# Kernel tuning notes

Hardware: AMD Instinct MI355X
Metric: run time of the kernel (lower is better)

## Reference

```python
import jax, jax.numpy as jnp
import numpy as np
import math

N, D, H, E = 4096, 128, 8, 131072
HD = D // H  # head_dim = 16
SCALE = 1.0 / math.sqrt(HD)


def ln(x, g, b, eps=1e-5):
    m = x.mean(-1, keepdims=True)
    v = ((x - m) ** 2).mean(-1, keepdims=True)
    return (x - m) * jax.lax.rsqrt(v + eps) * g + b


def setup_inputs() -> dict:
    key = jax.random.key(0)
    ks = iter(jax.random.split(key, 40))

    def lin(out_d, in_d):
        w = jax.random.normal(next(ks), (out_d, in_d), jnp.float32) / math.sqrt(in_d)
        b = jnp.zeros((out_d,), jnp.float32)
        return w, b

    x = jax.random.normal(next(ks), (N, D), jnp.float32)
    edge_index = jax.random.randint(next(ks), (2, E), 0, N, dtype=jnp.int64)
    wq_l, bq_l = lin(D, D); wk_l, bk_l = lin(D, D); wv_l, bv_l = lin(D, D)
    wg, bg = lin(D, 2 * D)
    wq_g, bq_g = lin(D, D); wk_g, bk_g = lin(D, D); wv_g, bv_g = lin(D, D)
    wo_g, bo_g = lin(D, D)
    wf, bf = lin(D, 2 * D)
    gf = jnp.ones((D,), jnp.float32); betaf = jnp.zeros((D,), jnp.float32)
    w1, b1 = lin(4 * D, D); w2, b2 = lin(D, 4 * D)
    g1 = jnp.ones((D,), jnp.float32); be1 = jnp.zeros((D,), jnp.float32)
    g2 = jnp.ones((D,), jnp.float32); be2 = jnp.zeros((D,), jnp.float32)
    return dict(x=x, edge_index=edge_index,
                wq_l=wq_l, bq_l=bq_l, wk_l=wk_l, bk_l=bk_l, wv_l=wv_l, bv_l=bv_l,
                wg=wg, bg=bg,
                wq_g=wq_g, bq_g=bq_g, wk_g=wk_g, bk_g=bk_g, wv_g=wv_g, bv_g=bv_g,
                wo_g=wo_g, bo_g=bo_g,
                wf=wf, bf=bf, gf=gf, betaf=betaf,
                w1=w1, b1=b1, w2=w2, b2=b2,
                g1=g1, be1=be1, g2=g2, be2=be2)


def reference(x, edge_index, wq_l, bq_l, wk_l, bk_l, wv_l, bv_l, wg, bg,
              wq_g, bq_g, wk_g, bk_g, wv_g, bv_g, wo_g, bo_g,
              wf, bf, gf, betaf, w1, b1, w2, b2, g1, be1, g2, be2):
    src, dst = edge_index[0], edge_index[1]  # PyG: j=source, i=target
    # ---- local edge-indexed multi-head attention (GraphInteractionModule) ----
    Q = (x @ wq_l.T + bq_l).reshape(N, H, HD)
    K = (x @ wk_l.T + bk_l).reshape(N, H, HD)
    V = (x @ wv_l.T + bv_l).reshape(N, H, HD)
    attn = (Q[dst] * K[src]).sum(-1) * SCALE            # [E, H]
    m = jax.ops.segment_max(attn, dst, num_segments=N)  # [N, H]
    e = jnp.exp(attn - m[dst])
    s = jax.ops.segment_sum(e, dst, num_segments=N)
    alpha = e / s[dst]                                  # segment softmax over edges into each dst
    agg = jax.ops.segment_sum(V[src] * alpha[..., None], dst, num_segments=N).reshape(N, D)
    gate = jax.nn.sigmoid(jnp.concatenate([x, agg], axis=-1) @ wg.T + bg)
    local = gate * agg + (1.0 - gate) * x
    # ---- global dense MHA over all nodes (B=1) ----
    xn = ln(x, g1, be1)
    q = (xn @ wq_g.T + bq_g).reshape(N, H, HD)
    k = (xn @ wk_g.T + bk_g).reshape(N, H, HD)
    v = (xn @ wv_g.T + bv_g).reshape(N, H, HD)
    scores = jnp.einsum('nhd,mhd->hnm', q, k) * SCALE   # [H, N, N]
    p = jax.nn.softmax(scores, axis=-1)
    go = jnp.einsum('hnm,mhd->nhd', p, v).reshape(N, D) @ wo_g.T + bo_g
    # ---- fusion + residual + FFN ----
    fused = jax.nn.relu(ln(jnp.concatenate([local, go], axis=-1) @ wf.T + bf, gf, betaf))
    h = x + fused
    h2 = ln(h, g2, be2)
    out = h + (jax.nn.gelu(h2 @ w1.T + b1, approximate=False) @ w2.T + b2)
    return out
```

## Files before the change

kernel.cpp:

```cpp
#include <hip/hip_runtime.h>
#include <math.h>

#define NN 4096
#define DM 128
#define NE 131072
#define BCAP 96
#define QSCALE 0.36067376022224085f
#define ESCALE 0.36067376022224085f

typedef short short8 __attribute__((ext_vector_type(8)));
typedef float f32x4  __attribute__((ext_vector_type(4)));
typedef unsigned int uint4v __attribute__((ext_vector_type(4)));

static __device__ __forceinline__ unsigned pk2(float lo, float hi) {
  union { float f; unsigned u; } a, b; a.f = lo; b.f = hi;
  return __builtin_amdgcn_perm(b.u + 0x8000u, a.u + 0x8000u, 0x07060302u);
}
static __device__ __forceinline__ unsigned pkp(float lo, float hi) {
  union { float f; unsigned u; } a, b; a.f = lo; b.f = hi;
  return __builtin_amdgcn_perm(b.u, a.u, 0x07060302u);
}
static __device__ __forceinline__ unsigned short f2bh(float f) {
  union { float f; unsigned u; } v; v.f = f;
  return (unsigned short)((v.u + 0x8000u) >> 16);
}
static __device__ __forceinline__ float b2f16(unsigned short u) {
  union { unsigned u; float f; } v; v.u = ((unsigned)u) << 16; return v.f;
}
static __device__ __forceinline__ float blo(unsigned u) {
  union { unsigned u; float f; } v; v.u = u << 16; return v.f;
}
static __device__ __forceinline__ float bhi(unsigned u) {
  union { unsigned u; float f; } v; v.u = u & 0xffff0000u; return v.f;
}
static __device__ __forceinline__ short8 cvt8(float4 a, float4 b) {
  uint4v u;
  u.x = pk2(a.x, a.y); u.y = pk2(a.z, a.w);
  u.z = pk2(b.x, b.y); u.w = pk2(b.z, b.w);
  return __builtin_bit_cast(short8, u);
}
static __device__ __forceinline__ int detect64(const int* __restrict__ EI) {
  int v = EI[2 * (threadIdx.x & 63) + 1];
  for (int off = 1; off < 64; off <<= 1) v |= __shfl_xor(v, off);
  return (v == 0) ? 1 : 0;
}

__global__ __launch_bounds__(256) void k_fill(float* __restrict__ out, float v, int n) {
  int i = blockIdx.x * 256 + threadIdx.x;
  if (i < n) out[i] = v;
}

#define LN1(V, GV, BV) V = (V - mean) * rstd * GV + BV
__global__ __launch_bounds__(256) void gemm_six(
    const float* __restrict__ X,
    const float* __restrict__ G1, const float* __restrict__ Be1,
    const float* __restrict__ W0, const float* __restrict__ W1, const float* __restrict__ W2,
    const float* __restrict__ W3, const float* __restrict__ W4, const float* __restrict__ W5,
    const float* __restrict__ B0, const float* __restrict__ B1, const float* __restrict__ B2,
    const float* __restrict__ B3, const float* __restrict__ B4, const float* __restrict__ B5,
    void* __restrict__ O0, void* __restrict__ O1, void* __restrict__ O2,
    void* __restrict__ O3, void* __restrict__ O4, void* __restrict__ O5,
    int* __restrict__ deg,
    const float* __restrict__ WFp, const float* __restrict__ WOg, const float* __restrict__ BOg,
    float* __restrict__ WCp, float* __restrict__ BFp)
{
  __shared__ short Asm[2][64][40];
  __shared__ short Wsm[2][64][40];
  if (blockIdx.y == 12) {
    if (blockIdx.x >= 16) return;
    const int c = threadIdx.x & 127;
    const int f0 = blockIdx.x * 8 + (threadIdx.x >> 7) * 4;
    const float* wf0 = WFp + (size_t)(f0 + 0) * 256 + 128;
    const float* wf1 = WFp + (size_t)(f0 + 1) * 256 + 128;
    const float* wf2 = WFp + (size_t)(f0 + 2) * 256 + 128;
    const float* wf3 = WFp + (size_t)(f0 + 3) * 256 + 128;
    float a0v = 0.f, a1v = 0.f, a2v = 0.f, a3v = 0.f;
    float c0 = 0.f, c1 = 0.f, c2 = 0.f, c3 = 0.f;
#pragma unroll 4
    for (int n = 0; n < 128; n++) {
      float wo = WOg[(size_t)n * 128 + c];
      float bv = BOg[n];
      float w0 = wf0[n], w1 = wf1[n], w2 = wf2[n], w3 = wf3[n];
      a0v += w0 * wo; a1v += w1 * wo; a2v += w2 * wo; a3v += w3 * wo;
      c0 += w0 * bv; c1 += w1 * bv; c2 += w2 * bv; c3 += w3 * bv;
    }
    WCp[(size_t)(f0 + 0) * 128 + c] = a0v;
    WCp[(size_t)(f0 + 1) * 128 + c] = a1v;
    WCp[(size_t)(f0 + 2) * 128 + c] = a2v;
    WCp[(size_t)(f0 + 3) * 128 + c] = a3v;
    if (c == 0) { BFp[f0] = c0; BFp[f0 + 1] = c1; BFp[f0 + 2] = c2; BFp[f0 + 3] = c3; }
    return;
  }
  if (blockIdx.x == 0 && blockIdx.y == 0) {
#pragma unroll
    for (int i = 0; i < 16; i++) deg[threadIdx.x * 16 + i] = 0;
  }
  const int g = blockIdx.y >> 1;
  const float* Wt  = (g==0)?W0:(g==1)?W1:(g==2)?W2:(g==3)?W3:(g==4)?W4:W5;
  const float* Bia = (g==0)?B0:(g==1)?B1:(g==2)?B2:(g==3)?B3:(g==4)?B4:B5;
  void* Cp         = (g==0)?O0:(g==1)?O1:(g==2)?O2:(g==3)?O3:(g==4)?O4:O5;
  const int omode  = (g==4)?3:(g==5)?2:1;
  const float osc  = (g==3)? QSCALE : (g==0)? ESCALE : 1.f;
  const int m0 = blockIdx.x * 64, n0 = (blockIdx.y & 1) * 64;
  const int tid = threadIdx.x;
  const int srow = tid >> 2, koff = (tid & 3) * 8;
  const int lane = tid & 63, wave = tid >> 6;
  const int quad = lane >> 4, m16 = lane & 15;

  const float* arow = X + (size_t)(m0 + srow) * 128 + koff;
  float4 a0[4], a1[4];
#pragma unroll
  for (int c = 0; c < 4; c++) {
    a0[c] = *(const float4*)(arow + c * 32);
    a1[c] = *(const float4*)(arow + c * 32 + 4);
  }
  if (g >= 3) {
    float s = 0.f;
#pragma unroll
    for (int c = 0; c < 4; c++)
      s += a0[c].x + a0[c].y + a0[c].z + a0[c].w + a1[c].x + a1[c].y + a1[c].z + a1[c].w;
    s += __shfl_xor(s, 1); s += __shfl_xor(s, 2);
    float mean = s * (1.0f / 128.0f);
    float v = 0.f;
#pragma unroll
    for (int c = 0; c < 4; c++) {
      float d;
      d = a0[c].x - mean; v += d*d;  d = a0[c].y - mean; v += d*d;
      d = a0[c].z - mean; v += d*d;  d = a0[c].w - mean; v += d*d;
      d = a1[c].x - mean; v += d*d;  d = a1[c].y - mean; v += d*d;
      d = a1[c].z - mean; v += d*d;  d = a1[c].w - mean; v += d*d;
    }
    v += __shfl_xor(v, 1); v += __shfl_xor(v, 2);
    float rstd = rsqrtf(v * (1.0f / 128.0f) + 1e-5f);
#pragma unroll
    for (int c = 0; c < 4; c++) {
      const int col = c * 32 + koff;
      float4 gv0 = *(const float4*)(G1 + col),  gv1 = *(const float4*)(G1 + col + 4);
      float4 bv0 = *(const float4*)(Be1 + col), bv1 = *(const float4*)(Be1 + col + 4);
      LN1(a0[c].x, gv0.x, bv0.x); LN1(a0[c].y, gv0.y, bv0.y);
      LN1(a0[c].z, gv0.z, bv0.z); LN1(a0[c].w, gv0.w, bv0.w);
      LN1(a1[c].x, gv1.x, bv1.x); LN1(a1[c].y, gv1.y, bv1.y);
      LN1(a1[c].z, gv1.z, bv1.z); LN1(a1[c].w, gv1.w, bv1.w);
    }
  }

  f32x4 acc[4];
#pragma unroll
  for (int i = 0; i < 4; i++) acc[i] = {0.f, 0.f, 0.f, 0.f};
  float4 w0r, w1r;
  {
    const float* wp = Wt + (size_t)(n0 + srow) * 128 + koff;
    w0r = *(const float4*)wp; w1r = *(const float4*)(wp + 4);
  }
#pragma unroll
  for (int c = 0; c < 4; c++) {
    const int cur = c & 1;
    *(short8*)&Asm[cur][srow][koff] = cvt8(a0[c], a1[c]);
    *(short8*)&Wsm[cur][srow][koff] = cvt8(w0r, w1r);
    __syncthreads();
    if (c < 3) {
      const float* wp = Wt + (size_t)(n0 + srow) * 128 + (c + 1) * 32 + koff;
      w0r = *(const float4*)wp; w1r = *(const float4*)(wp + 4);
    }
    short8 af = *(short8*)&Asm[cur][wave * 16 + m16][quad * 8];
#pragma unroll
    for (int nt = 0; nt < 4; nt++) {
      short8 bf = *(short8*)&Wsm[cur][nt * 16 + m16][quad * 8];
      acc[nt] = __builtin_amdgcn_mfma_f32_16x16x32_bf16(af, bf, acc[nt], 0, 0, 0);
    }
  }
#pragma unroll
  for (int nt = 0; nt < 4; nt++) {
#pragma unroll
    for (int r = 0; r < 4; r++) {
      const int m = m0 + wave * 16 + quad * 4 + r;
      const int n = n0 + nt * 16 + m16;
      float v = (acc[nt][r] + Bia[n]) * osc;
      size_t oi = (size_t)m * 128 + n;
      if (omode == 1)      ((unsigned short*)Cp)[oi] = f2bh(v);
      else if (omode == 3) ((unsigned short*)Cp)[(size_t)(n >> 4) * (NN * 16) + (size_t)m * 16 + (n & 15)] = f2bh(v);
      else                 ((unsigned short*)Cp)[(size_t)n * NN + m] = f2bh(v);
    }
  }
}

__global__ __launch_bounds__(512) void k_attn_fused(
    const unsigned short* __restrict__ Kh, const unsigned short* __restrict__ Qb,
    const unsigned short* __restrict__ VT, float* __restrict__ O,
    const int* __restrict__ EI, const unsigned short* __restrict__ Qb16,
    const unsigned short* __restrict__ Kb16,
    unsigned short* __restrict__ EB, int* __restrict__ deg, int* __restrict__ EL)
{
  __shared__ float LO[8][4][16][16];
  __shared__ float LL[8][4][16];
  if (blockIdx.x >= 512) {
    int is64 = detect64(EI);
    int gid = (blockIdx.x - 512) * 512 + threadIdx.x;
    int e = gid >> 3, hh = gid & 7;
    int s = is64 ? EI[2*e]      : EI[e];
    int d = is64 ? EI[2*(NE+e)] : EI[NE+e];
    s = min(max(s, 0), NN-1); d = min(max(d, 0), NN-1);
    const uint4v* qp = (const uint4v*)(Qb16 + (size_t)d * DM + hh * 16);
    const uint4v* kp = (const uint4v*)(Kb16 + (size_t)s * DM + hh * 16);
    uint4v qa = qp[0], qb2 = qp[1];
    uint4v ka = kp[0], kb2 = kp[1];
    float acc = 0.f;
#pragma unroll
    for (int i2 = 0; i2 < 4; i2++) {
      acc += blo(qa[i2]) * blo(ka[i2]) + bhi(qa[i2]) * bhi(ka[i2]);
      acc += blo(qb2[i2]) * blo(kb2[i2]) + bhi(qb2[i2]) * bhi(kb2[i2]);
    }
    EB[(size_t)e*8 + hh] = f2bh(__builtin_amdgcn_exp2f(fminf(acc, 43.0f)));
    if (hh == 0) {
      int slot = atomicAdd(&deg[d], 1);
      if (slot < BCAP) EL[d * BCAP + slot] = e;
    }
    return;
  }
  const int h = blockIdx.x >> 6, qt = blockIdx.x & 63;
  const int tid = threadIdx.x, lane = tid & 63, wave = tid >> 6;
  const int quad = lane >> 4, m16 = lane & 15;
  const int r0 = qt * 64;
  const short8 z8 = {0,0,0,0,0,0,0,0};
  const f32x4  z4 = {0.f,0.f,0.f,0.f};
  short8 qf[4] = {z8, z8, z8, z8};
  if (quad < 2) {
#pragma unroll
    for (int j = 0; j < 4; j++)
      qf[j] = *(const short8*)(Qb + (size_t)(r0 + j * 16 + m16) * DM + h * 16 + quad * 8);
  }
  short8 ones;
#pragma unroll
  for (int i = 0; i < 8; i++) ones[i] = (short)0x3F80;
  const int kperm = (m16 >> 2) * 8 + (m16 & 3);
  const int kbase = wave * 512;
  const unsigned short* khead = Kh + (size_t)h * (NN * 16);
  f32x4 acc[4] = {z4, z4, z4, z4};
  f32x4 acc2[4] = {z4, z4, z4, z4};
  short8 a0 = z8, a1 = z8, a2 = z8, a3 = z8;
  for (int kt = 0; kt < 8; kt++) {
    const int key0 = kbase + kt * 64;
    if (quad < 2) {
      const unsigned short* kp = khead + (size_t)(key0 + kperm) * 16 + quad * 8;
      a0 = *(const short8*)kp;
      a1 = *(const short8*)(kp + 4 * 16);
      a2 = *(const short8*)(kp + 32 * 16);
      a3 = *(const short8*)(kp + 36 * 16);
    }
    const unsigned short* vp = VT + (size_t)(h * 16 + m16) * NN + key0 + quad * 8;
    short8 av0 = *(const short8*)vp;
    short8 av1 = *(const short8*)(vp + 32);
#pragma unroll
    for (int j = 0; j < 4; j++) {
      f32x4 s0 = __builtin_amdgcn_mfma_f32_16x16x32_bf16(a0, qf[j], z4, 0, 0, 0);
      f32x4 s1 = __builtin_amdgcn_mfma_f32_16x16x32_bf16(a1, qf[j], z4, 0, 0, 0);
      f32x4 s2 = __builtin_amdgcn_mfma_f32_16x16x32_bf16(a2, qf[j], z4, 0, 0, 0);
      f32x4 s3 = __builtin_amdgcn_mfma_f32_16x16x32_bf16(a3, qf[j], z4, 0, 0, 0);
      float e0 = __builtin_amdgcn_exp2f(s0[0]), e1 = __builtin_amdgcn_exp2f(s0[1]);
      float e2 = __builtin_amdgcn_exp2f(s0[2]), e3 = __builtin_amdgcn_exp2f(s0[3]);
      float e4 = __builtin_amdgcn_exp2f(s1[0]), e5 = __builtin_amdgcn_exp2f(s1[1]);
      float e6 = __builtin_amdgcn_exp2f(s1[2]), e7 = __builtin_amdgcn_exp2f(s1[3]);
      uint4v u;
      u.x = pkp(e0, e1); u.y = pkp(e2, e3); u.z = pkp(e4, e5); u.w = pkp(e6, e7);
      short8 p0 = __builtin_bit_cast(short8, u);
      float f0 = __builtin_amdgcn_exp2f(s2[0]), f1 = __builtin_amdgcn_exp2f(s2[1]);
      float f2 = __builtin_amdgcn_exp2f(s2[2]), f3 = __builtin_amdgcn_exp2f(s2[3]);
      float f4 = __builtin_amdgcn_exp2f(s3[0]), f5 = __builtin_amdgcn_exp2f(s3[1]);
      float f6 = __builtin_amdgcn_exp2f(s3[2]), f7 = __builtin_amdgcn_exp2f(s3[3]);
      uint4v w;
      w.x = pkp(f0, f1); w.y = pkp(f2, f3); w.z = pkp(f4, f5); w.w = pkp(f6, f7);
      short8 p1 = __builtin_bit_cast(short8, w);
      acc[j]  = __builtin_amdgcn_mfma_f32_16x16x32_bf16(av0, p0, acc[j], 0, 0, 0);
      acc[j]  = __builtin_amdgcn_mfma_f32_16x16x32_bf16(av1, p1, acc[j], 0, 0, 0);
      acc2[j] = __builtin_amdgcn_mfma_f32_16x16x32_bf16(ones, p0, acc2[j], 0, 0, 0);
      acc2[j] = __builtin_amdgcn_mfma_f32_16x16x32_bf16(ones, p1, acc2[j], 0, 0, 0);
    }
  }
#pragma unroll
  for (int j = 0; j < 4; j++) {
    float4 a4; a4.x = acc[j][0]; a4.y = acc[j][1]; a4.z = acc[j][2]; a4.w = acc[j][3];
    *(float4*)&LO[wave][j][m16][quad * 4] = a4;
    if (lane < 16) LL[wave][j][lane] = acc2[j][0];
  }
  __syncthreads();
  if (wave < 4) {
    const int j = wave;
    float4 o = *(float4*)&LO[0][j][m16][quad * 4];
    float lt = LL[0][j][m16];
#pragma unroll
    for (int w2 = 1; w2 < 8; w2++) {
      float4 t = *(float4*)&LO[w2][j][m16][quad * 4];
      o.x += t.x; o.y += t.y; o.z += t.z; o.w += t.w;
      lt += LL[w2][j][m16];
    }
    float inv = 1.0f / fmaxf(lt, 1e-30f);
    float4 r4; r4.x = o.x * inv; r4.y = o.y * inv; r4.z = o.z * inv; r4.w = o.w * inv;
    *(float4*)(O + (size_t)(r0 + j * 16 + m16) * DM + h * 16 + quad * 4) = r4;
  }
}

__global__ __launch_bounds__(256) void k_edge_agg3(const int* __restrict__ EI,
    const int* __restrict__ deg,
    const int* __restrict__ elist, const unsigned short* __restrict__ Vl,
    const unsigned short* __restrict__ EB, float* __restrict__ AG) {
  __shared__ float PS[2][128];
  __shared__ float SSH[2][2][8];
  int is64 = detect64(EI);
  int tid = threadIdx.x;
  int dsti = tid >> 7;
  int half = (tid >> 6) & 1;
  int lane = tid & 63;
  int d = blockIdx.x * 2 + dsti;
  int degd = min(deg[d], BCAP), start = d * BCAP;
  int hh = lane >> 3;
  float ss = 0.f;
  for (int i = (lane & 7) * 2 + half; i < degd; i += 16)
    ss += b2f16(EB[(size_t)elist[start + i] * 8 + hh]);
  for (int o = 1; o < 8; o <<= 1) ss += __shfl_xor(ss, o);
  if ((lane & 7) == 0) SSH[dsti][half][hh] = ss;
  __syncthreads();
  float inv = 1.0f / fmaxf(SSH[dsti][0][hh] + SSH[dsti][1][hh], 1e-30f);
  float ax = 0.f, ay = 0.f;
  int i = half;
  for (; i + 6 < degd; i += 8) {
    int e0 = elist[start+i], e1 = elist[start+i+2], e2 = elist[start+i+4], e3 = elist[start+i+6];
    int s0 = is64 ? EI[2*e0] : EI[e0];
    int s1 = is64 ? EI[2*e1] : EI[e1];
    int s2 = is64 ? EI[2*e2] : EI[e2];
    int s3 = is64 ? EI[2*e3] : EI[e3];
    s0 = min(max(s0,0),NN-1); s1 = min(max(s1,0),NN-1);
    s2 = min(max(s2,0),NN-1); s3 = min(max(s3,0),NN-1);
    float w0 = b2f16(EB[(size_t)e0*8 + hh]) * inv;
    float w1 = b2f16(EB[(size_t)e1*8 + hh]) * inv;
    float w2 = b2f16(EB[(size_t)e2*8 + hh]) * inv;
    float w3 = b2f16(EB[(size_t)e3*8 + hh]) * inv;
    unsigned v0 = *(const unsigned*)(Vl + (size_t)s0 * DM + 2 * lane);
    unsigned v1 = *(const unsigned*)(Vl + (size_t)s1 * DM + 2 * lane);
    unsigned v2 = *(const unsigned*)(Vl + (size_t)s2 * DM + 2 * lane);
    unsigned v3 = *(const unsigned*)(Vl + (size_t)s3 * DM + 2 * lane);
    ax += w0 * b2f16((unsigned short)(v0 & 0xffffu)) + w1 * b2f16((unsigned short)(v1 & 0xffffu))
        + w2 * b2f16((unsigned short)(v2 & 0xffffu)) + w3 * b2f16((unsigned short)(v3 & 0xffffu));
    ay += w0 * b2f16((unsigned short)(v0 >> 16)) + w1 * b2f16((unsigned short)(v1 >> 16))
        + w2 * b2f16((unsigned short)(v2 >> 16)) + w3 * b2f16((unsigned short)(v3 >> 16));
  }
  for (; i < degd; i += 2) {
    int e = elist[start + i];
    int s = is64 ? EI[2*e] : EI[e];
    s = min(max(s, 0), NN-1);
    float a = b2f16(EB[(size_t)e*8 + hh]) * inv;
    unsigned v = *(const unsigned*)(Vl + (size_t)s * DM + 2 * lane);
    ax += a * b2f16((unsigned short)(v & 0xffffu));
    ay += a * b2f16((unsigned short)(v >> 16));
  }
  if (half == 1) { PS[dsti][2*lane] = ax; PS[dsti][2*lane+1] = ay; }
  __syncthreads();
  if (half == 0) {
    float2 r; r.x = ax + PS[dsti][2*lane]; r.y = ay + PS[dsti][2*lane+1];
    *(float2*)(AG + (size_t)d * DM + 2 * lane) = r;
  }
}

__global__ __launch_bounds__(256) void gemm_gatefuse(
    const float* __restrict__ X, const float* __restrict__ AGG, const float* __restrict__ GO,
    const float* __restrict__ Wg, const float* __restrict__ Bg,
    const float* __restrict__ WF, const float* __restrict__ WC,
    const float* __restrict__ BF, const float* __restrict__ BFOLD,
    float* __restrict__ TMPF)
{
  __shared__ short Asm[64][40];
  __shared__ short Wsm[128][40];
  __shared__ short Lsm[4][64][40];
  const int m0 = blockIdx.x * 64, n0 = blockIdx.y * 64;
  const int tid = threadIdx.x;
  const int srow = tid >> 2, koff = (tid & 3) * 8;
  const int wrow = tid >> 1, koff2 = (tid & 1) * 16;
  const int lane = tid & 63, wave = tid >> 6;
  const int quad = lane >> 4, m16 = lane & 15;

  f32x4 acc8[8];
#pragma unroll
  for (int i = 0; i < 8; i++) acc8[i] = {0.f, 0.f, 0.f, 0.f};
  for (int k0 = 0; k0 < 256; k0 += 32) {
    const int kg = k0 + koff;
    const float* ap = (kg < 128) ? (X + (size_t)(m0 + srow) * 128 + kg)
                                 : (AGG + (size_t)(m0 + srow) * 128 + (kg - 128));
    float4 a0 = *(const float4*)ap, a1 = *(const float4*)(ap + 4);
    const float* wp = Wg + (size_t)wrow * 256 + k0 + koff2;
    float4 w0 = *(const float4*)wp,       w1v = *(const float4*)(wp + 4);
    float4 w2v = *(const float4*)(wp + 8), w3v = *(const float4*)(wp + 12);
    __syncthreads();
    *(short8*)&Asm[srow][koff] = cvt8(a0, a1);
    *(short8*)&Wsm[wrow][koff2]     = cvt8(w0, w1v);
    *(short8*)&Wsm[wrow][koff2 + 8] = cvt8(w2v, w3v);
    __syncthreads();
    short8 af = *(short8*)&Asm[wave * 16 + m16][quad * 8];
#pragma unroll
    for (int nt = 0; nt < 8; nt++) {
      short8 bf = *(short8*)&Wsm[nt * 16 + m16][quad * 8];
      acc8[nt] = __builtin_amdgcn_mfma_f32_16x16x32_bf16(af, bf, acc8[nt], 0, 0, 0);
    }
  }
  __syncthreads();
#pragma unroll
  for (int nt = 0; nt < 8; nt++) {
#pragma unroll
    for (int r = 0; r < 4; r++) {
      const int mr = wave * 16 + quad * 4 + r;
      const int n = nt * 16 + m16;
      float v = acc8[nt][r] + Bg[n];
      size_t oi = (size_t)(m0 + mr) * 128 + n;
      float gg = 1.0f / (1.0f + __expf(fminf(fmaxf(-v, -80.f), 80.f)));
      float loc = gg * AGG[oi] + (1.0f - gg) * X[oi];
      Lsm[n >> 5][mr][n & 31] = (short)f2bh(loc);
    }
  }

  f32x4 acc[4];
#pragma unroll
  for (int i = 0; i < 4; i++) acc[i] = {0.f, 0.f, 0.f, 0.f};
  for (int k0 = 0; k0 < 256; k0 += 32) {
    const int c = k0 >> 5;
    float4 a0g, a1g;
    if (c >= 4) {
      const float* ap = GO + (size_t)(m0 + srow) * 128 + (k0 - 128) + koff;
      a0g = *(const float4*)ap; a1g = *(const float4*)(ap + 4);
    }
    const float* wp = (c < 4) ? (WF + (size_t)(n0 + srow) * 256 + k0 + koff)
                              : (WC + (size_t)(n0 + srow) * 128 + (k0 - 128) + koff);
    float4 w0 = *(const float4*)wp, w1v = *(const float4*)(wp + 4);
    __syncthreads();
    if (c >= 4) *(short8*)&Asm[srow][koff] = cvt8(a0g, a1g);
    *(short8*)&Wsm[srow][koff] = cvt8(w0, w1v);
    __syncthreads();
    short8 af = (c < 4) ? *(short8*)&Lsm[c][wave * 16 + m16][quad * 8]
                        : *(short8*)&Asm[wave * 16 + m16][quad * 8];
#pragma unroll
    for (int nt = 0; nt < 4; nt++) {
      short8 bf = *(short8*)&Wsm[nt * 16 + m16][quad * 8];
      acc[nt] = __builtin_amdgcn_mfma_f32_16x16x32_bf16(af, bf, acc[nt], 0, 0, 0);
    }
  }
#pragma unroll
  for (int nt = 0; nt < 4; nt++) {
#pragma unroll
    for (int r = 0; r < 4; r++) {
      const int m = m0 + wave * 16 + quad * 4 + r;
      const int n = n0 + nt * 16 + m16;
      TMPF[(size_t)m * 128 + n] = acc[nt][r] + BF[n] + BFOLD[n];
    }
  }
}

__global__ __launch_bounds__(256) void gemm_ffn1(
    const float* __restrict__ T, const float* __restrict__ X,
    const float* __restrict__ Gf, const float* __restrict__ Bef,
    const float* __restrict__ G2, const float* __restrict__ Be2,
    const float* __restrict__ W1, const float* __restrict__ B1,
    float* __restrict__ H, unsigned short* __restrict__ T1)
{
  __shared__ short Asm[2][64][40];
  __shared__ short Wsm[2][64][40];
  const int m0 = blockIdx.x * 64, n0 = blockIdx.y * 64;
  const int tid = threadIdx.x;
  const int srow = tid >> 2, koff = (tid & 3) * 8;
  const int lane = tid & 63, wave = tid >> 6;
  const int quad = lane >> 4, m16 = lane & 15;

  const float* trow = T + (size_t)(m0 + srow) * 128 + koff;
  const float* xrow = X + (size_t)(m0 + srow) * 128 + koff;
  float4 a0[4], a1[4];
#pragma unroll
  for (int c = 0; c < 4; c++) {
    a0[c] = *(const float4*)(trow + c * 32);
    a1[c] = *(const float4*)(trow + c * 32 + 4);
  }
  {
    float s = 0.f;
#pragma unroll
    for (int c = 0; c < 4; c++)
      s += a0[c].x + a0[c].y + a0[c].z + a0[c].w + a1[c].x + a1[c].y + a1[c].z + a1[c].w;
    s += __shfl_xor(s, 1); s += __shfl_xor(s, 2);
    float mean = s * (1.0f / 128.0f);
    float v = 0.f;
#pragma unroll
    for (int c = 0; c < 4; c++) {
      float d;
      d = a0[c].x - mean; v += d*d;  d = a0[c].y - mean; v += d*d;
      d = a0[c].z - mean; v += d*d;  d = a0[c].w - mean; v += d*d;
      d = a1[c].x - mean; v += d*d;  d = a1[c].y - mean; v += d*d;
      d = a1[c].z - mean; v += d*d;  d = a1[c].w - mean; v += d*d;
    }
    v += __shfl_xor(v, 1); v += __shfl_xor(v, 2);
    float rstd = rsqrtf(v * (1.0f / 128.0f) + 1e-5f);
#pragma unroll
    for (int c = 0; c < 4; c++) {
      const int col = c * 32 + koff;
      float4 gv0 = *(const float4*)(Gf + col),  gv1 = *(const float4*)(Gf + col + 4);
      float4 bv0 = *(const float4*)(Bef + col), bv1 = *(const float4*)(Bef + col + 4);
      float4 x0 = *(const float4*)(xrow + c * 32), x1 = *(const float4*)(xrow + c * 32 + 4);
      LN1(a0[c].x, gv0.x, bv0.x); LN1(a0[c].y, gv0.y, bv0.y);
      LN1(a0[c].z, gv0.z, bv0.z); LN1(a0[c].w, gv0.w, bv0.w);
      LN1(a1[c].x, gv1.x, bv1.x); LN1(a1[c].y, gv1.y, bv1.y);
      LN1(a1[c].z, gv1.z, bv1.z); LN1(a1[c].w, gv1.w, bv1.w);
      a0[c].x = x0.x + fmaxf(a0[c].x, 0.f); a0[c].y = x0.y + fmaxf(a0[c].y, 0.f);
      a0[c].z = x0.z + fmaxf(a0[c].z, 0.f); a0[c].w = x0.w + fmaxf(a0[c].w, 0.f);
      a1[c].x = x1.x + fmaxf(a1[c].x, 0.f); a1[c].y = x1.y + fmaxf(a1[c].y, 0.f);
      a1[c].z = x1.z + fmaxf(a1[c].z, 0.f); a1[c].w = x1.w + fmaxf(a1[c].w, 0.f);
      if (blockIdx.y == 0) {
        *(float4*)(H + (size_t)(m0 + srow) * 128 + c * 32 + koff)     = a0[c];
        *(float4*)(H + (size_t)(m0 + srow) * 128 + c * 32 + koff + 4) = a1[c];
      }
    }
  }
  {
    float s = 0.f;
#pragma unroll
    for (int c = 0; c < 4; c++)
      s += a0[c].x + a0[c].y + a0[c].z + a0[c].w + a1[c].x + a1[c].y + a1[c].z + a1[c].w;
    s += __shfl_xor(s, 1); s += __shfl_xor(s, 2);
    float mean = s * (1.0f / 128.0f);
    float v = 0.f;
#pragma unroll
    for (int c = 0; c < 4; c++) {
      float d;
      d = a0[c].x - mean; v += d*d;  d = a0[c].y - mean; v += d*d;
      d = a0[c].z - mean; v += d*d;  d = a0[c].w - mean; v += d*d;
      d = a1[c].x - mean; v += d*d;  d = a1[c].y - mean; v += d*d;
      d = a1[c].z - mean; v += d*d;  d = a1[c].w - mean; v += d*d;
    }
    v += __shfl_xor(v, 1); v += __shfl_xor(v, 2);
    float rstd = rsqrtf(v * (1.0f / 128.0f) + 1e-5f);
#pragma unroll
    for (int c = 0; c < 4; c++) {
      const int col = c * 32 + koff;
      float4 gv0 = *(const float4*)(G2 + col),  gv1 = *(const float4*)(G2 + col + 4);
      float4 bv0 = *(const float4*)(Be2 + col), bv1 = *(const float4*)(Be2 + col + 4);
      LN1(a0[c].x, gv0.x, bv0.x); LN1(a0[c].y, gv0.y, bv0.y);
      LN1(a0[c].z, gv0.z, bv0.z); LN1(a0[c].w, gv0.w, bv0.w);
      LN1(a1[c].x, gv1.x, bv1.x); LN1(a1[c].y, gv1.y, bv1.y);
      LN1(a1[c].z, gv1.z, bv1.z); LN1(a1[c].w, gv1.w, bv1.w);
    }
  }

  f32x4 acc[4];
#pragma unroll
  for (int i = 0; i < 4; i++) acc[i] = {0.f, 0.f, 0.f, 0.f};
  float4 w0r, w1r;
  {
    const float* wp = W1 + (size_t)(n0 + srow) * 128 + koff;
    w0r = *(const float4*)wp; w1r = *(const float4*)(wp + 4);
  }
#pragma unroll
  for (int c = 0; c < 4; c++) {
    const int cur = c & 1;
    *(short8*)&Asm[cur][srow][koff] = cvt8(a0[c], a1[c]);
    *(short8*)&Wsm[cur][srow][koff] = cvt8(w0r, w1r);
    __syncthreads();
    if (c < 3) {
      const float* wp = W1 + (size_t)(n0 + srow) * 128 + (c + 1) * 32 + koff;
      w0r = *(const float4*)wp; w1r = *(const float4*)(wp + 4);
    }
    short8 af = *(short8*)&Asm[cur][wave * 16 + m16][quad * 8];
#pragma unroll
    for (int nt = 0; nt < 4; nt++) {
      short8 bf = *(short8*)&Wsm[cur][nt * 16 + m16][quad * 8];
      acc[nt] = __builtin_amdgcn_mfma_f32_16x16x32_bf16(af, bf, acc[nt], 0, 0, 0);
    }
  }
#pragma unroll
  for (int nt = 0; nt < 4; nt++) {
#pragma unroll
    for (int r = 0; r < 4; r++) {
      const int m = m0 + wave * 16 + quad * 4 + r;
      const int n = n0 + nt * 16 + m16;
      float v = acc[nt][r] + B1[n];
      v = 0.5f * v * (1.0f + erff(v * 0.70710678118654752f));
      T1[(size_t)m * 512 + n] = f2bh(v);
    }
  }
}

__global__ __launch_bounds__(256) void gemm_w2b(
    const unsigned short* __restrict__ A,
    const float* __restrict__ Wt, const float* __restrict__ Bias,
    const float* __restrict__ Res, float* __restrict__ Cp)
{
  __shared__ short Asm[2][64][40];
  __shared__ short Wsm[2][64][40];
  const int m0 = blockIdx.x * 64, n0 = blockIdx.y * 64;
  const int tid = threadIdx.x;
  const int srow = tid >> 2, koff = (tid & 3) * 8;
  const int lane = tid & 63, wave = tid >> 6;
  const int quad = lane >> 4, m16 = lane & 15;
  f32x4 acc[4];
#pragma unroll
  for (int i = 0; i < 4; i++) acc[i] = {0.f, 0.f, 0.f, 0.f};

  short8 avr; float4 w0r, w1r;
  {
    avr = *(const short8*)(A + (size_t)(m0 + srow) * 512 + koff);
    const float* wp = Wt + (size_t)(n0 + srow) * 512 + koff;
    w0r = *(const float4*)wp; w1r = *(const float4*)(wp + 4);
  }
  for (int k0 = 0; k0 < 512; k0 += 32) {
    const int cur = (k0 >> 5) & 1;
    *(short8*)&Asm[cur][srow][koff] = avr;
    *(short8*)&Wsm[cur][srow][koff] = cvt8(w0r, w1r);
    __syncthreads();
    if (k0 + 32 < 512) {
      const int kg = k0 + 32 + koff;
      avr = *(const short8*)(A + (size_t)(m0 + srow) * 512 + kg);
      const float* wp = Wt + (size_t)(n0 + srow) * 512 + kg;
      w0r = *(const float4*)wp; w1r = *(const float4*)(wp + 4);
    }
    short8 af = *(short8*)&Asm[cur][wave * 16 + m16][quad * 8];
#pragma unroll
    for (int nt = 0; nt < 4; nt++) {
      short8 bf = *(short8*)&Wsm[cur][nt * 16 + m16][quad * 8];
      acc[nt] = __builtin_amdgcn_mfma_f32_16x16x32_bf16(af, bf, acc[nt], 0, 0, 0);
    }
  }
#pragma unroll
  for (int nt = 0; nt < 4; nt++) {
#pragma unroll
    for (int r = 0; r < 4; r++) {
      const int m = m0 + wave * 16 + quad * 4 + r;
      const int n = n0 + nt * 16 + m16;
      size_t oi = (size_t)m * 128 + n;
      Cp[oi] = acc[nt][r] + Bias[n] + Res[oi];
    }
  }
}

extern "C" void kernel_launch(void* const* d_in, const int* in_sizes, int n_in,
                              void* d_out, int out_size, void* d_ws, size_t ws_size,
                              hipStream_t stream) {
  const float* x     = (const float*)d_in[0];
  const int*   ei    = (const int*)  d_in[1];
  const float* wq_l  = (const float*)d_in[2];  const float* bq_l = (const float*)d_in[3];
  const float* wk_l  = (const float*)d_in[4];  const float* bk_l = (const float*)d_in[5];
  const float* wv_l  = (const float*)d_in[6];  const float* bv_l = (const float*)d_in[7];
  const float* wg    = (const float*)d_in[8];  const float* bg   = (const float*)d_in[9];
  const float* wq_g  = (const float*)d_in[10]; const float* bq_g = (const float*)d_in[11];
  const float* wk_g  = (const float*)d_in[12]; const float* bk_g = (const float*)d_in[13];
  const float* wv_g  = (const float*)d_in[14]; const float* bv_g = (const float*)d_in[15];
  const float* wo_g  = (const float*)d_in[16]; const float* bo_g = (const float*)d_in[17];
  const float* wf    = (const float*)d_in[18]; const float* bff  = (const float*)d_in[19];
  const float* gf    = (const float*)d_in[20]; const float* betaf= (const float*)d_in[21];
  const float* w1    = (const float*)d_in[22]; const float* b1   = (const float*)d_in[23];
  const float* w2    = (const float*)d_in[24]; const float* b2   = (const float*)d_in[25];
  const float* g1    = (const float*)d_in[26]; const float* be1  = (const float*)d_in[27];
  const float* g2    = (const float*)d_in[28]; const float* be2  = (const float*)d_in[29];
  float* out = (float*)d_out;

  const size_t NEED = (size_t)3698816 * 4;
  if (ws_size < NEED) {
    k_fill<<<2048, 256, 0, stream>>>(out, 100.0f, NN*DM);
    return;
  }

  float* W = (float*)d_ws;
  unsigned short* lQb   = (unsigned short*)(W + 0);
  unsigned short* lKb   = (unsigned short*)(W + 524288);
  unsigned short* lV    = (unsigned short*)(W + 1048576);
  unsigned short* eb    = (unsigned short*)(W + 1310720);
  float*          go    = W + 1835008;
  unsigned short* qgb   = (unsigned short*)(W + 2359296);
  unsigned short* kgb   = (unsigned short*)(W + 2621440);
  unsigned short* vgT   = (unsigned short*)(W + 2883584);
  float*          agg   = W + 0;
  float*          tmpf  = W + 1310720;
  float*          h     = W + 2621440;
  unsigned short* t1    = (unsigned short*)(W + 0);
  int* deg    = (int*)(W + 3145728);
  float* Wc    = W + 3289088;
  float* bfold = W + 3305472;
  int* elist96 = (int*)(W + 3305600);

  dim3 b256(256);

  gemm_six<<<dim3(64,13), b256, 0, stream>>>(x, g1, be1,
      wq_l, wk_l, wv_l, wq_g, wk_g, wv_g,
      bq_l, bk_l, bv_l, bq_g, bk_g, bv_g,
      lQb, lKb, lV, qgb, kgb, vgT, deg,
      wf, wo_g, bo_g, Wc, bfold);

  k_attn_fused<<<2560, dim3(512), 0, stream>>>(kgb, qgb, vgT, go, ei, lQb, lKb, eb, deg, elist96);

  k_edge_agg3<<<2048, b256, 0, stream>>>(ei, deg, elist96, lV, eb, agg);

  gemm_gatefuse<<<dim3(64,2), b256, 0, stream>>>(x, agg, go, wg, bg, wf, Wc, bff, bfold, tmpf);
  gemm_ffn1<<<dim3(64,8), b256, 0, stream>>>(tmpf, x, gf, betaf, g2, be2, w1, b1, h, t1);
  gemm_w2b<<<dim3(64,2), b256, 0, stream>>>(t1, w2, b2, h, out);
}
```

Baseline: 208.2 us.

## Move edge score computation into the destination-grouped aggregation kernel

The per-edge QK dot product and exp moves out of the attention kernel's extra blocks and into k_edge_agg3. Scores are computed per destination with the dst Q row held in registers, reduced across 8 lanes with shuffles, and kept in shared memory, so the global EB buffer write and re-read go away. The attention kernel's side blocks now only build the adjacency lists, each thread handling four edges, which shrinks the grid from 2560 to 576 blocks. In exchange, K rows are gathered by destination inside the aggregation kernel, which adds a dependent gather pass and shared-memory use there, and agg moves to a new workspace region that raises the required size.

New measurement: 207.7 us. About the same (-0.3%).

```diff
diff --git a/kernel.cpp b/kernel.cpp
--- a/kernel.cpp
+++ b/kernel.cpp
@@ -187,31 +187,18 @@
 __global__ __launch_bounds__(512) void k_attn_fused(
     const unsigned short* __restrict__ Kh, const unsigned short* __restrict__ Qb,
     const unsigned short* __restrict__ VT, float* __restrict__ O,
-    const int* __restrict__ EI, const unsigned short* __restrict__ Qb16,
-    const unsigned short* __restrict__ Kb16,
-    unsigned short* __restrict__ EB, int* __restrict__ deg, int* __restrict__ EL)
+    const int* __restrict__ EI, int* __restrict__ deg, int* __restrict__ EL)
 {
   __shared__ float LO[8][4][16][16];
   __shared__ float LL[8][4][16];
   if (blockIdx.x >= 512) {
     int is64 = detect64(EI);
-    int gid = (blockIdx.x - 512) * 512 + threadIdx.x;
-    int e = gid >> 3, hh = gid & 7;
-    int s = is64 ? EI[2*e]      : EI[e];
-    int d = is64 ? EI[2*(NE+e)] : EI[NE+e];
-    s = min(max(s, 0), NN-1); d = min(max(d, 0), NN-1);
-    const uint4v* qp = (const uint4v*)(Qb16 + (size_t)d * DM + hh * 16);
-    const uint4v* kp = (const uint4v*)(Kb16 + (size_t)s * DM + hh * 16);
-    uint4v qa = qp[0], qb2 = qp[1];
-    uint4v ka = kp[0], kb2 = kp[1];
-    float acc = 0.f;
-#pragma unroll
-    for (int i2 = 0; i2 < 4; i2++) {
-      acc += blo(qa[i2]) * blo(ka[i2]) + bhi(qa[i2]) * bhi(ka[i2]);
-      acc += blo(qb2[i2]) * blo(kb2[i2]) + bhi(qb2[i2]) * bhi(kb2[i2]);
-    }
-    EB[(size_t)e*8 + hh] = f2bh(__builtin_amdgcn_exp2f(fminf(acc, 43.0f)));
-    if (hh == 0) {
+    int base = (blockIdx.x - 512) * 2048 + threadIdx.x;
+#pragma unroll
+    for (int r = 0; r < 4; r++) {
+      int e = base + r * 512;
+      int d = is64 ? EI[2*(NE+e)] : EI[NE+e];
+      d = min(max(d, 0), NN-1);
       int slot = atomicAdd(&deg[d], 1);
       if (slot < BCAP) EL[d * BCAP + slot] = e;
     }
@@ -300,11 +287,12 @@
 }
 
 __global__ __launch_bounds__(256) void k_edge_agg3(const int* __restrict__ EI,
-    const int* __restrict__ deg,
-    const int* __restrict__ elist, const unsigned short* __restrict__ Vl,
-    const unsigned short* __restrict__ EB, float* __restrict__ AG) {
+    const int* __restrict__ deg, const int* __restrict__ elist,
+    const unsigned short* __restrict__ Vl, const unsigned short* __restrict__ Kb,
+    const unsigned short* __restrict__ Qb, float* __restrict__ AG) {
   __shared__ float PS[2][128];
   __shared__ float SSH[2][2][8];
+  __shared__ float SC[2][BCAP][8];
   int is64 = detect64(EI);
   int tid = threadIdx.x;
   int dsti = tid >> 7;
@@ -313,44 +301,89 @@
   int d = blockIdx.x * 2 + dsti;
   int degd = min(deg[d], BCAP), start = d * BCAP;
   int hh = lane >> 3;
+  unsigned qv = *(const unsigned*)(Qb + (size_t)d * DM + 2 * lane);
+  float q0 = blo(qv), q1 = bhi(qv);
   float ss = 0.f;
-  for (int i = (lane & 7) * 2 + half; i < degd; i += 16)
-    ss += b2f16(EB[(size_t)elist[start + i] * 8 + hh]);
-  for (int o = 1; o < 8; o <<= 1) ss += __shfl_xor(ss, o);
-  if ((lane & 7) == 0) SSH[dsti][half][hh] = ss;
-  __syncthreads();
-  float inv = 1.0f / fmaxf(SSH[dsti][0][hh] + SSH[dsti][1][hh], 1e-30f);
-  float ax = 0.f, ay = 0.f;
   int i = half;
   for (; i + 6 < degd; i += 8) {
     int e0 = elist[start+i], e1 = elist[start+i+2], e2 = elist[start+i+4], e3 = elist[start+i+6];
+    e0 = min(max(e0,0),NE-1); e1 = min(max(e1,0),NE-1);
+    e2 = min(max(e2,0),NE-1); e3 = min(max(e3,0),NE-1);
     int s0 = is64 ? EI[2*e0] : EI[e0];
     int s1 = is64 ? EI[2*e1] : EI[e1];
     int s2 = is64 ? EI[2*e2] : EI[e2];
     int s3 = is64 ? EI[2*e3] : EI[e3];
     s0 = min(max(s0,0),NN-1); s1 = min(max(s1,0),NN-1);
     s2 = min(max(s2,0),NN-1); s3 = min(max(s3,0),NN-1);
-    float w0 = b2f16(EB[(size_t)e0*8 + hh]) * inv;
-    float w1 = b2f16(EB[(size_t)e1*8 + hh]) * inv;
-    float w2 = b2f16(EB[(size_t)e2*8 + hh]) * inv;
-    float w3 = b2f16(EB[(size_t)e3*8 + hh]) * inv;
+    unsigned k0 = *(const unsigned*)(Kb + (size_t)s0 * DM + 2 * lane);
+    unsigned k1 = *(const unsigned*)(Kb + (size_t)s1 * DM + 2 * lane);
+    unsigned k2 = *(const unsigned*)(Kb + (size_t)s2 * DM + 2 * lane);
+    unsigned k3 = *(const unsigned*)(Kb + (size_t)s3 * DM + 2 * lane);
+    float p0 = q0 * blo(k0) + q1 * bhi(k0);
+    float p1 = q0 * blo(k1) + q1 * bhi(k1);
+    float p2 = q0 * blo(k2) + q1 * bhi(k2);
+    float p3 = q0 * blo(k3) + q1 * bhi(k3);
+    p0 += __shfl_xor(p0,1); p0 += __shfl_xor(p0,2); p0 += __shfl_xor(p0,4);
+    p1 += __shfl_xor(p1,1); p1 += __shfl_xor(p1,2); p1 += __shfl_xor(p1,4);
+    p2 += __shfl_xor(p2,1); p2 += __shfl_xor(p2,2); p2 += __shfl_xor(p2,4);
+    p3 += __shfl_xor(p3,1); p3 += __shfl_xor(p3,2); p3 += __shfl_xor(p3,4);
+    float ev0 = __builtin_amdgcn_exp2f(fminf(p0, 43.0f));
+    float ev1 = __builtin_amdgcn_exp2f(fminf(p1, 43.0f));
+    float ev2 = __builtin_amdgcn_exp2f(fminf(p2, 43.0f));
+    float ev3 = __builtin_amdgcn_exp2f(fminf(p3, 43.0f));
+    if ((lane & 7) == 0) {
+      SC[dsti][i][hh] = ev0;   SC[dsti][i+2][hh] = ev1;
+      SC[dsti][i+4][hh] = ev2; SC[dsti][i+6][hh] = ev3;
+    }
+    ss += ev0 + ev1 + ev2 + ev3;
+  }
+  for (; i < degd; i += 2) {
+    int e = elist[start + i];
+    e = min(max(e,0),NE-1);
+    int s = is64 ? EI[2*e] : EI[e];
+    s = min(max(s, 0), NN-1);
+    unsigned k = *(const unsigned*)(Kb + (size_t)s * DM + 2 * lane);
+    float p = q0 * blo(k) + q1 * bhi(k);
+    p += __shfl_xor(p,1); p += __shfl_xor(p,2); p += __shfl_xor(p,4);
+    float ev = __builtin_amdgcn_exp2f(fminf(p, 43.0f));
+    if ((lane & 7) == 0) SC[dsti][i][hh] = ev;
+    ss += ev;
+  }
+  if ((lane & 7) == 0) SSH[dsti][half][hh] = ss;
+  __syncthreads();
+  float inv = 1.0f / fmaxf(SSH[dsti][0][hh] + SSH[dsti][1][hh], 1e-30f);
+  float ax = 0.f, ay = 0.f;
+  i = half;
+  for (; i + 6 < degd; i += 8) {
+    int e0 = elist[start+i], e1 = elist[start+i+2], e2 = elist[start+i+4], e3 = elist[start+i+6];
+    e0 = min(max(e0,0),NE-1); e1 = min(max(e1,0),NE-1);
+    e2 = min(max(e2,0),NE-1); e3 = min(max(e3,0),NE-1);
+    int s0 = is64 ? EI[2*e0] : EI[e0];
+    int s1 = is64 ? EI[2*e1] : EI[e1];
+    int s2 = is64 ? EI[2*e2] : EI[e2];
+    int s3 = is64 ? EI[2*e3] : EI[e3];
+    s0 = min(max(s0,0),NN-1); s1 = min(max(s1,0),NN-1);
+    s2 = min(max(s2,0),NN-1); s3 = min(max(s3,0),NN-1);
+    float w0 = SC[dsti][i][hh] * inv;
+    float w1 = SC[dsti][i+2][hh] * inv;
+    float w2 = SC[dsti][i+4][hh] * inv;
+    float w3 = SC[dsti][i+6][hh] * inv;
     unsigned v0 = *(const unsigned*)(Vl + (size_t)s0 * DM + 2 * lane);
     unsigned v1 = *(const unsigned*)(Vl + (size_t)s1 * DM + 2 * lane);
     unsigned v2 = *(const unsigned*)(Vl + (size_t)s2 * DM + 2 * lane);
     unsigned v3 = *(const unsigned*)(Vl + (size_t)s3 * DM + 2 * lane);
-    ax += w0 * b2f16((unsigned short)(v0 & 0xffffu)) + w1 * b2f16((unsigned short)(v1 & 0xffffu))
-        + w2 * b2f16((unsigned short)(v2 & 0xffffu)) + w3 * b2f16((unsigned short)(v3 & 0xffffu));
-    ay += w0 * b2f16((unsigned short)(v0 >> 16)) + w1 * b2f16((unsigned short)(v1 >> 16))
-        + w2 * b2f16((unsigned short)(v2 >> 16)) + w3 * b2f16((unsigned short)(v3 >> 16));
+    ax += w0 * blo(v0) + w1 * blo(v1) + w2 * blo(v2) + w3 * blo(v3);
+    ay += w0 * bhi(v0) + w1 * bhi(v1) + w2 * bhi(v2) + w3 * bhi(v3);
   }
   for (; i < degd; i += 2) {
     int e = elist[start + i];
+    e = min(max(e,0),NE-1);
     int s = is64 ? EI[2*e] : EI[e];
     s = min(max(s, 0), NN-1);
-    float a = b2f16(EB[(size_t)e*8 + hh]) * inv;
+    float a = SC[dsti][i][hh] * inv;
     unsigned v = *(const unsigned*)(Vl + (size_t)s * DM + 2 * lane);
-    ax += a * b2f16((unsigned short)(v & 0xffffu));
-    ay += a * b2f16((unsigned short)(v >> 16));
+    ax += a * blo(v);
+    ay += a * bhi(v);
   }
   if (half == 1) { PS[dsti][2*lane] = ax; PS[dsti][2*lane+1] = ay; }
   __syncthreads();
@@ -653,7 +686,7 @@
   const float* g2    = (const float*)d_in[28]; const float* be2  = (const float*)d_in[29];
   float* out = (float*)d_out;
 
-  const size_t NEED = (size_t)3698816 * 4;
+  const size_t NEED = (size_t)4223104 * 4;
   if (ws_size < NEED) {
     k_fill<<<2048, 256, 0, stream>>>(out, 100.0f, NN*DM);
     return;
@@ -663,12 +696,10 @@
   unsigned short* lQb   = (unsigned short*)(W + 0);
   unsigned short* lKb   = (unsigned short*)(W + 524288);
   unsigned short* lV    = (unsigned short*)(W + 1048576);
-  unsigned short* eb    = (unsigned short*)(W + 1310720);
   float*          go    = W + 1835008;
   unsigned short* qgb   = (unsigned short*)(W + 2359296);
   unsigned short* kgb   = (unsigned short*)(W + 2621440);
   unsigned short* vgT   = (unsigned short*)(W + 2883584);
-  float*          agg   = W + 0;
   float*          tmpf  = W + 1310720;
   float*          h     = W + 2621440;
   unsigned short* t1    = (unsigned short*)(W + 0);
@@ -676,6 +707,7 @@
   float* Wc    = W + 3289088;
   float* bfold = W + 3305472;
   int* elist96 = (int*)(W + 3305600);
+  float*          agg   = W + 3698816;
 
   dim3 b256(256);
 
@@ -685,9 +717,9 @@
       lQb, lKb, lV, qgb, kgb, vgT, deg,
       wf, wo_g, bo_g, Wc, bfold);
 
-  k_attn_fused<<<2560, dim3(512), 0, stream>>>(kgb, qgb, vgT, go, ei, lQb, lKb, eb, deg, elist96);
-
-  k_edge_agg3<<<2048, b256, 0, stream>>>(ei, deg, elist96, lV, eb, agg);
+  k_attn_fused<<<576, dim3(512), 0, stream>>>(kgb, qgb, vgT, go, ei, deg, elist96);
+
+  k_edge_agg3<<<2048, b256, 0, stream>>>(ei, deg, elist96, lV, lKb, lQb, agg);
 
   gemm_gatefuse<<<dim3(64,2), b256, 0, stream>>>(x, agg, go, wg, bg, wf, Wc, bff, bfold, tmpf);
   gemm_ffn1<<<dim3(64,8), b256, 0, stream>>>(tmpf, x, gf, betaf, g2, be2, w1, b1, h, t1);
```
